# Kernel optimization log

Hardware: AMD Instinct MI355X
Metric: run time of the kernel (lower is better)

## Reference

```python
import jax, jax.numpy as jnp
import numpy as np
import math

B, S, DIM, H = 4, 1024, 4096, 32
HD = DIM // H  # head_dim = 128
MAX_B, MAX_S = 4, 1024
START_POS = 0
ROPE_THETA = 10000.0


def setup_inputs() -> dict:
    key = jax.random.key(0)
    ks = jax.random.split(key, 6)
    x = jax.random.normal(ks[0], (B, S, DIM), dtype=jnp.float32)
    # real RoPE frequencies: freqs_cis[t, j] = exp(i * t * theta^{-2j/hd})
    inv_freq = 1.0 / (ROPE_THETA ** (jnp.arange(0, HD, 2, dtype=jnp.float32) / HD))  # [HD/2]
    t = jnp.arange(START_POS, START_POS + S, dtype=jnp.float32)
    ang = jnp.outer(t, inv_freq)  # [S, HD/2]
    freqs_cos = jnp.cos(ang)
    freqs_sin = jnp.sin(ang)
    # additive causal mask as in llama: -inf above diagonal offset start_pos+1
    mask = jnp.triu(jnp.full((1, 1, S, S), float('-inf'), dtype=jnp.float32), k=START_POS + 1)
    scale = 0.02
    wq = jax.random.normal(ks[1], (DIM, DIM), dtype=jnp.float32) * scale
    wk = jax.random.normal(ks[2], (DIM, DIM), dtype=jnp.float32) * scale
    wv = jax.random.normal(ks[3], (DIM, DIM), dtype=jnp.float32) * scale
    wo = jax.random.normal(ks[4], (DIM, DIM), dtype=jnp.float32) * scale
    cache_k = jnp.zeros((MAX_B, MAX_S, H, HD), dtype=jnp.float32)
    cache_v = jnp.zeros((MAX_B, MAX_S, H, HD), dtype=jnp.float32)
    return {"x": x, "start_pos": START_POS, "freqs_cos": freqs_cos, "freqs_sin": freqs_sin,
            "mask": mask, "wq": wq, "wk": wk, "wv": wv, "wo": wo,
            "cache_k": cache_k, "cache_v": cache_v}


def _apply_rotary(t, cos, sin):
    # t: [B, S, H, HD]; interpret last dim as HD/2 complex pairs (real, imag)
    b, s, h, d = t.shape
    tr = t.reshape(b, s, h, d // 2, 2)
    a, bb = tr[..., 0], tr[..., 1]
    c = cos[None, :, None, :]  # [1, S, 1, HD/2]
    si = sin[None, :, None, :]
    out_r = a * c - bb * si
    out_i = a * si + bb * c
    return jnp.stack([out_r, out_i], axis=-1).reshape(b, s, h, d)


def reference(x, start_pos, freqs_cos, freqs_sin, mask, wq, wk, wv, wo, cache_k, cache_v):
    bsz, seqlen, dim = x.shape
    hd = HD
    # torch Linear: y = x @ W.T, W is [out, in]
    xq = (x @ wq.T).reshape(bsz, seqlen, H, hd)
    xk = (x @ wk.T).reshape(bsz, seqlen, H, hd)
    xv = (x @ wv.T).reshape(bsz, seqlen, H, hd)
    xq = _apply_rotary(xq, freqs_cos, freqs_sin)
    xk = _apply_rotary(xk, freqs_cos, freqs_sin)
    # KV-cache write
    cache_k = jax.lax.dynamic_update_slice(cache_k, xk, (0, start_pos, 0, 0))
    cache_v = jax.lax.dynamic_update_slice(cache_v, xv, (0, start_pos, 0, 0))
    keys = cache_k[:bsz, :start_pos + seqlen]    # [B, K, H, HD]
    values = cache_v[:bsz, :start_pos + seqlen]  # [B, K, H, HD]
    # naive attention: full score matrix
    scores = jnp.einsum('bqhd,bkhd->bhqk', xq, keys) / math.sqrt(hd)
    scores = scores + mask
    probs = jax.nn.softmax(scores.astype(jnp.float32), axis=-1).astype(xq.dtype)
    out = jnp.einsum('bhqk,bkhd->bqhd', probs, values)
    out = out.reshape(bsz, seqlen, -1)
    return out @ wo.T
```

## Files before the change

kernel.cpp:

```cpp
#include <hip/hip_runtime.h>
#include <hip/hip_bf16.h>
#include <cstdint>

typedef __hip_bfloat16 bf16;
typedef __attribute__((ext_vector_type(8))) short frag8;
typedef __attribute__((ext_vector_type(4))) float f32x4;

#define DEV __device__ __forceinline__

DEV void gl_lds16(const void* g, void* l) {
  __builtin_amdgcn_global_load_lds(
      (const __attribute__((address_space(1))) void*)g,
      (__attribute__((address_space(3))) void*)l, 16, 0, 0);
}

DEV void storeC(float* C, size_t idx, float v) { C[idx] = v; }
DEV void storeC(bf16* C, size_t idx, float v) { C[idx] = __float2bfloat16(v); }

__global__ __launch_bounds__(256) void conv_all(const float* __restrict__ x,
                                                const float* __restrict__ wq,
                                                const float* __restrict__ wk,
                                                const float* __restrict__ wv,
                                                const float* __restrict__ wo,
                                                bf16* __restrict__ xb, bf16* __restrict__ qb,
                                                bf16* __restrict__ kb, bf16* __restrict__ vb,
                                                bf16* __restrict__ ob) {
  const float* src;
  bf16* dst;
  switch (blockIdx.y) {
    case 0: src = x;  dst = xb; break;
    case 1: src = wq; dst = qb; break;
    case 2: src = wk; dst = kb; break;
    case 3: src = wv; dst = vb; break;
    default: src = wo; dst = ob; break;
  }
  int i = blockIdx.x * 256 + threadIdx.x;
  const f32x4* in4 = reinterpret_cast<const f32x4*>(src);
  f32x4 a = __builtin_nontemporal_load(in4 + 2 * i);
  f32x4 b = __builtin_nontemporal_load(in4 + 2 * i + 1);
  union { frag8 v; bf16 h[8]; } u;
  u.h[0] = __float2bfloat16(a.x); u.h[1] = __float2bfloat16(a.y);
  u.h[2] = __float2bfloat16(a.z); u.h[3] = __float2bfloat16(a.w);
  u.h[4] = __float2bfloat16(b.x); u.h[5] = __float2bfloat16(b.y);
  u.h[6] = __float2bfloat16(b.z); u.h[7] = __float2bfloat16(b.w);
  __builtin_nontemporal_store(u.v, reinterpret_cast<frag8*>(dst + (size_t)i * 8));
}

#define MF(a, b, c) __builtin_amdgcn_mfma_f32_16x16x32_bf16(a, b, c, 0, 0, 0)

#define STAGE(isB, h, tt, bp) do {                                             \
    char* _d = lds + ((isB) * 65536) + ((((bp) * 2) + (h)) << 14);             \
    gl_lds16(((isB) ? gB : gA)[h][0] + (size_t)(tt) * 64, _d + ldsOff0);       \
    gl_lds16(((isB) ? gB : gA)[h][1] + (size_t)(tt) * 64, _d + ldsOff1);       \
  } while (0)

#define RDA(mi, ckk) (*(const frag8*)(ab + aRowB + (mi) * 2048 + (ckk)))
#define RDB(ni, ckk) (*(const frag8*)(bb + bRowB + (ni) * 2048 + (ckk)))

#define PHASE(p, SSTAGE, SWAIT) do {                                           \
    if ((p) == 0) {                                                            \
      b00 = RDB(0, ck0); b01 = RDB(0, ck1); b10 = RDB(1, ck0); b11 = RDB(1, ck1); \
      b20 = RDB(2, ck0); b21 = RDB(2, ck1); b30 = RDB(3, ck0); b31 = RDB(3, ck1); \
    }                                                                          \
    frag8 a00 = RDA(2 * (p), ck0), a01 = RDA(2 * (p), ck1);                    \
    frag8 a10 = RDA(2 * (p) + 1, ck0), a11 = RDA(2 * (p) + 1, ck1);            \
    SSTAGE;                                                                    \
    SWAIT;                                                                     \
    __builtin_amdgcn_s_barrier();                                              \
    __builtin_amdgcn_s_setprio(1);                                             \
    acc[2*(p)][0]   = MF(a00, b00, acc[2*(p)][0]);                             \
    acc[2*(p)][1]   = MF(a00, b10, acc[2*(p)][1]);                             \
    acc[2*(p)][2]   = MF(a00, b20, acc[2*(p)][2]);                             \
    acc[2*(p)][3]   = MF(a00, b30, acc[2*(p)][3]);                             \
    acc[2*(p)+1][0] = MF(a10, b00, acc[2*(p)+1][0]);                           \
    acc[2*(p)+1][1] = MF(a10, b10, acc[2*(p)+1][1]);                           \
    acc[2*(p)+1][2] = MF(a10, b20, acc[2*(p)+1][2]);                           \
    acc[2*(p)+1][3] = MF(a10, b30, acc[2*(p)+1][3]);                           \
    acc[2*(p)][0]   = MF(a01, b01, acc[2*(p)][0]);                             \
    acc[2*(p)][1]   = MF(a01, b11, acc[2*(p)][1]);                             \
    acc[2*(p)][2]   = MF(a01, b21, acc[2*(p)][2]);                             \
    acc[2*(p)][3]   = MF(a01, b31, acc[2*(p)][3]);                             \
    acc[2*(p)+1][0] = MF(a11, b01, acc[2*(p)+1][0]);                           \
    acc[2*(p)+1][1] = MF(a11, b11, acc[2*(p)+1][1]);                           \
    acc[2*(p)+1][2] = MF(a11, b21, acc[2*(p)+1][2]);                           \
    acc[2*(p)+1][3] = MF(a11, b31, acc[2*(p)+1][3]);                           \
    __builtin_amdgcn_s_setprio(0);                                             \
    __builtin_amdgcn_s_barrier();                                              \
  } while (0)

#define VM4 asm volatile("s_waitcnt vmcnt(4)" ::: "memory")
#define VM0 asm volatile("s_waitcnt vmcnt(0)" ::: "memory")
#define NOW ((void)0)

#define TILE(t, SA, SB, SWAIT) do {                                            \
    const int _bp2 = ((t) & 1) * 2;                                            \
    char* ab = lds + ((_bp2 + wm) << 14);                                      \
    char* bb = lds + 65536 + ((_bp2 + bhalf) << 14);                           \
    PHASE(0, { if (SA) STAGE(0, 0, (t) + 1, ((t) + 1) & 1); }, NOW);           \
    PHASE(1, { if (SA) STAGE(0, 1, (t) + 1, ((t) + 1) & 1); }, NOW);           \
    PHASE(2, { if (SB) STAGE(1, 0, (t) + 2, (t) & 1); }, NOW);                 \
    PHASE(3, { if (SB) STAGE(1, 1, (t) + 2, (t) & 1); }, SWAIT);               \
  } while (0)

template <typename OutT, int EPI>
__global__ __launch_bounds__(512, 2) void gemm8(const bf16* __restrict__ A,
                                                const bf16* __restrict__ Bt,
                                                OutT* __restrict__ C,
                                                const float* __restrict__ fc,
                                                const float* __restrict__ fs,
                                                float oscale) {
  __shared__ __align__(16) char lds[131072];
  const int K = 4096, N = 4096;
  const int t = threadIdx.x;
  const int lane = t & 63, w = t >> 6;
  const int wm = w >> 2, wn = w & 3;
  const int lr = lane & 15, lg = lane >> 4;
  const int bhalf = wn >> 1;

  const int bid = blockIdx.x;
  const int wg = (bid & 7) * 32 + (bid >> 3);
  const int m0 = (wg >> 4) * 256, n0 = (wg & 15) * 256;

  const bf16* gA[2][2];
  const bf16* gB[2][2];
  int ldsOff0, ldsOff1;
  {
    int c0 = (w * 2 + 0) * 64 + lane;
    int c1 = (w * 2 + 1) * 64 + lane;
    int r0 = c0 >> 3, r1 = c1 >> 3;
    int e0 = ((c0 & 7) ^ (r0 & 7)) * 8;
    int e1 = ((c1 & 7) ^ (r1 & 7)) * 8;
    ldsOff0 = c0 * 16; ldsOff1 = c1 * 16;
    gA[0][0] = A + (size_t)(m0 + r0) * K + e0;
    gA[0][1] = A + (size_t)(m0 + r1) * K + e1;
    gA[1][0] = A + (size_t)(m0 + 128 + r0) * K + e0;
    gA[1][1] = A + (size_t)(m0 + 128 + r1) * K + e1;
    gB[0][0] = Bt + (size_t)(n0 + r0) * K + e0;
    gB[0][1] = Bt + (size_t)(n0 + r1) * K + e1;
    gB[1][0] = Bt + (size_t)(n0 + 128 + r0) * K + e0;
    gB[1][1] = Bt + (size_t)(n0 + 128 + r1) * K + e1;
  }

  const int swz = (lr & 7) << 4;
  const int ck0 = (lg * 16) ^ swz;
  const int ck1 = (64 + lg * 16) ^ swz;
  const int aRowB = lr * 128;
  const int bRowB = ((wn & 1) * 64 + lr) * 128;

  f32x4 acc[8][4];
#pragma unroll
  for (int mi = 0; mi < 8; ++mi)
#pragma unroll
    for (int ni = 0; ni < 4; ++ni) acc[mi][ni] = (f32x4){0.f, 0.f, 0.f, 0.f};

  frag8 b00, b01, b10, b11, b20, b21, b30, b31;

  STAGE(1, 0, 0, 0); STAGE(1, 1, 0, 0);
  STAGE(0, 0, 0, 0); STAGE(0, 1, 0, 0);
  STAGE(1, 0, 1, 1); STAGE(1, 1, 1, 1);
  VM4;
  __builtin_amdgcn_s_barrier();

  for (int tt = 0; tt < 62; tt += 2) {
    TILE(tt, 1, 1, VM4);
    TILE(tt + 1, 1, 1, VM4);
  }
  TILE(62, 1, 0, VM0);
  TILE(63, 0, 0, NOW);

#pragma unroll
  for (int mi = 0; mi < 8; ++mi)
#pragma unroll
    for (int ni = 0; ni < 4; ++ni) {
      f32x4 v = acc[mi][ni];
      int col = n0 + wn * 64 + ni * 16 + lr;
      if (EPI == 1) {
        int i = (col & 127) >> 1;
        const bool odd = (col & 1);
#pragma unroll
        for (int ii = 0; ii < 4; ++ii) {
          int row = m0 + wm * 128 + mi * 16 + lg * 4 + ii;
          int s = row & 1023;
          float c = fc[s * 64 + i], si = fs[s * 64 + i];
          float val = v[ii];
          float par = __shfl_xor(val, 1);
          float o = (val * c + (odd ? par * si : -par * si)) * oscale;
          storeC(C, (size_t)row * N + col, o);
        }
      } else if (EPI == 2) {
        int row0 = m0 + wm * 128 + mi * 16 + lg * 4;
        size_t base = ((size_t)(row0 >> 10) * 4096 + col) * 1024 + (row0 & 1023);
        union { ushort4 s4; unsigned short us[4]; } pk;
#pragma unroll
        for (int ii = 0; ii < 4; ++ii) {
          union { bf16 b; unsigned short u; } cv;
          cv.b = __float2bfloat16(v[ii]);
          pk.us[ii] = cv.u;
        }
        *reinterpret_cast<ushort4*>(reinterpret_cast<bf16*>(C) + base) = pk.s4;
      } else {
#pragma unroll
        for (int ii = 0; ii < 4; ++ii) {
          int row = m0 + wm * 128 + mi * 16 + lg * 4 + ii;
          storeC(C, (size_t)row * N + col, v[ii]);
        }
      }
    }
}

__global__ __launch_bounds__(512, 4) void attn_kernel(const bf16* __restrict__ q,
                                                      const bf16* __restrict__ k,
                                                      const bf16* __restrict__ vt,
                                                      bf16* __restrict__ out) {
  __shared__ __align__(16) char als[81920];
  const int qt = 7 - blockIdx.x, h = blockIdx.y, b = blockIdx.z;
  const int t = threadIdx.x;
  const int lane = t & 63, w = t >> 6;
  const int lr = lane & 15, lg = lane >> 4;
  const int NT = 2 * qt + 2;

  frag8 aq[4];
  {
    const bf16* qp = q + ((size_t)(b * 1024 + qt * 128 + w * 16 + lr)) * 4096 + h * 128 + lg * 8;
#pragma unroll
    for (int ks = 0; ks < 4; ++ks) aq[ks] = *reinterpret_cast<const frag8*>(qp + ks * 32);
  }

  const bf16* kbase = k + (size_t)b * 1024 * 4096 + h * 128;
  const bf16* vbase = vt + ((size_t)(b * 32 + h)) * 128 * 1024;

  const int L0 = t * 16, L1 = (t + 512) * 16;
  const int kr0 = L0 >> 8, kr1 = L1 >> 8;
  const size_t kOff0 = (size_t)kr0 * 4096 + (((L0 & 255) ^ ((kr0 & 7) << 4)) >> 1);
  const size_t kOff1 = (size_t)kr1 * 4096 + (((L1 & 255) ^ ((kr1 & 7) << 4)) >> 1);
  const int vr0 = L0 >> 7, vr1 = L1 >> 7;
  const size_t vOff0 = (size_t)vr0 * 1024 + (((L0 & 127) ^ ((vr0 & 7) << 4)) >> 1);
  const size_t vOff1 = (size_t)vr1 * 1024 + (((L1 & 127) ^ ((vr1 & 7) << 4)) >> 1);

#define STAGE_K(tt, bp) do { char* _d = als + (bp) * 16384;                    \
    gl_lds16(kbase + (size_t)(tt) * 262144 + kOff0, _d + L0);                  \
    gl_lds16(kbase + (size_t)(tt) * 262144 + kOff1, _d + L1); } while (0)
#define STAGE_V(tt, bp) do { char* _d = als + 32768 + (bp) * 16384;            \
    gl_lds16(vbase + (size_t)(tt) * 64 + vOff0, _d + L0);                      \
    gl_lds16(vbase + (size_t)(tt) * 64 + vOff1, _d + L1); } while (0)

  f32x4 oacc[8] = {};
  float mrow = -1e30f, lrow = 0.f;
  char* Pw = als + 65536 + w * 2048;
  const int qmaxw = qt * 128 + w * 16 + 15;
  const int qr_g = qt * 128 + w * 16 + lr;

  STAGE_K(0, 0); STAGE_V(0, 0);
  STAGE_K(1, 1); STAGE_V(1, 1);

  for (int kt = 0; kt < NT; ++kt) {
    const int cur = kt & 1;
    const bool act = (kt * 64 <= qmaxw);
    const bool domask = (kt >= 2 * qt);
    char* Kc = als + cur * 16384;
    char* Vc = als + 32768 + cur * 16384;

    if (kt + 1 < NT) { VM4; } else { VM0; }
    __builtin_amdgcn_s_barrier();

    f32x4 sacc[4] = {};
    if (act) {
      __builtin_amdgcn_s_setprio(1);
#pragma unroll
      for (int ks = 0; ks < 4; ++ks) {
#pragma unroll
        for (int ni = 0; ni < 4; ++ni) {
          int n = ni * 16 + lr;
          frag8 bk = *reinterpret_cast<const frag8*>(
              Kc + n * 256 + ((ks * 64 + lg * 16) ^ ((n & 7) << 4)));
          sacc[ni] = MF(bk, aq[ks], sacc[ni]);
        }
      }
      __builtin_amdgcn_s_setprio(0);
    }
    __builtin_amdgcn_s_barrier();
    if (kt + 2 < NT) STAGE_K(kt + 2, cur);

    if (act) {
      if (domask) {
#pragma unroll
        for (int ni = 0; ni < 4; ++ni)
#pragma unroll
          for (int i = 0; i < 4; ++i) {
            int kc = kt * 64 + ni * 16 + lg * 4 + i;
            if (kc > qr_g) sacc[ni][i] = -1e30f;
          }
      }

      float pm = sacc[0][0];
#pragma unroll
      for (int ni = 0; ni < 4; ++ni)
#pragma unroll
        for (int i = 0; i < 4; ++i) pm = fmaxf(pm, sacc[ni][i]);
      pm = fmaxf(pm, __shfl_xor(pm, 16));
      pm = fmaxf(pm, __shfl_xor(pm, 32));
      const bool skip = __all(pm <= mrow + 8.f);
      float mn, f;
      if (skip) { mn = mrow; f = 1.f; }
      else      { mn = fmaxf(mrow, pm); f = __expf(mrow - mn); mrow = mn; }
      float rs = 0.f;
#pragma unroll
      for (int ni = 0; ni < 4; ++ni)
#pragma unroll
        for (int i = 0; i < 4; ++i) {
          float p = __expf(sacc[ni][i] - mn);
          sacc[ni][i] = p;
          rs += p;
        }
      rs += __shfl_xor(rs, 16);
      rs += __shfl_xor(rs, 32);
      lrow = lrow * f + rs;

#pragma unroll
      for (int ni = 0; ni < 4; ++ni)
#pragma unroll
        for (int jj = 0; jj < 2; ++jj) {
          union { uint32_t u; bf16 hh[2]; } pk;
          pk.hh[0] = __float2bfloat16(sacc[ni][2 * jj]);
          pk.hh[1] = __float2bfloat16(sacc[ni][2 * jj + 1]);
          int kc2 = (ni * 16 + lg * 4 + 2 * jj) * 2;
          *reinterpret_cast<uint32_t*>(Pw + lr * 128 + (kc2 ^ ((lr & 7) << 4))) = pk.u;
        }

      if (!skip) {
        float fi0 = __shfl(f, lg * 4 + 0);
        float fi1 = __shfl(f, lg * 4 + 1);
        float fi2 = __shfl(f, lg * 4 + 2);
        float fi3 = __shfl(f, lg * 4 + 3);
#pragma unroll
        for (int nj = 0; nj < 8; ++nj) {
          oacc[nj][0] *= fi0; oacc[nj][1] *= fi1;
          oacc[nj][2] *= fi2; oacc[nj][3] *= fi3;
        }
      }

      __builtin_amdgcn_s_setprio(1);
#pragma unroll
      for (int ks2 = 0; ks2 < 2; ++ks2) {
        frag8 ap = *reinterpret_cast<const frag8*>(
            Pw + lr * 128 + ((ks2 * 64 + lg * 16) ^ ((lr & 7) << 4)));
#pragma unroll
        for (int nj = 0; nj < 8; ++nj) {
          int d = nj * 16 + lr;
          frag8 bv = *reinterpret_cast<const frag8*>(
              Vc + d * 128 + ((ks2 * 64 + lg * 16) ^ ((d & 7) << 4)));
          oacc[nj] = MF(ap, bv, oacc[nj]);
        }
      }
      __builtin_amdgcn_s_setprio(0);
    }
    __builtin_amdgcn_s_barrier();
    if (kt + 2 < NT) STAGE_V(kt + 2, cur);
  }

  float lv0 = __shfl(lrow, lg * 4 + 0);
  float lv1 = __shfl(lrow, lg * 4 + 1);
  float lv2 = __shfl(lrow, lg * 4 + 2);
  float lv3 = __shfl(lrow, lg * 4 + 3);
#pragma unroll
  for (int nj = 0; nj < 8; ++nj) {
    int srow0 = qt * 128 + w * 16 + lg * 4;
    size_t base = ((size_t)(b * 1024 + srow0)) * 4096 + h * 128 + nj * 16 + lr;
    out[base]          = __float2bfloat16(oacc[nj][0] / lv0);
    out[base + 4096]   = __float2bfloat16(oacc[nj][1] / lv1);
    out[base + 8192]   = __float2bfloat16(oacc[nj][2] / lv2);
    out[base + 12288]  = __float2bfloat16(oacc[nj][3] / lv3);
  }
#undef STAGE_K
#undef STAGE_V
}

extern "C" void kernel_launch(void* const* d_in, const int* in_sizes, int n_in,
                              void* d_out, int out_size, void* d_ws, size_t ws_size,
                              hipStream_t stream) {
  const float* x  = (const float*)d_in[0];
  const float* fc = (const float*)d_in[2];
  const float* fs = (const float*)d_in[3];
  const float* wq = (const float*)d_in[5];
  const float* wk = (const float*)d_in[6];
  const float* wv = (const float*)d_in[7];
  const float* wo = (const float*)d_in[8];
  float* out = (float*)d_out;

  const size_t SZ = (size_t)4096 * 4096 * 2;
  char* w = (char*)d_ws;
  bf16* xb  = (bf16*)(w);
  bf16* wbq = (bf16*)(w + SZ);
  bf16* qb  = (bf16*)(w + 2 * SZ);
  bf16* kb  = (bf16*)(w + 3 * SZ);
  bf16* vtb = (bf16*)(w + 4 * SZ);
  bf16* wbk = (bf16*)(w + 5 * SZ);
  bf16* wbv = (bf16*)(w + 6 * SZ);
  bf16* wbo = (bf16*)(w + 7 * SZ);
  bf16* ao  = xb;

  const int n8 = 4096 * 4096 / 8;
  dim3 cgrd(n8 / 256, 5), blk(256);
  dim3 ggrd(256);
  dim3 gblk(512);

  conv_all<<<cgrd, blk, 0, stream>>>(x, wq, wk, wv, wo, xb, wbq, wbk, wbv, wbo);
  gemm8<bf16, 1><<<ggrd, gblk, 0, stream>>>(xb, wbq, qb, fc, fs, 0.08838834764831845f);
  gemm8<bf16, 1><<<ggrd, gblk, 0, stream>>>(xb, wbk, kb, fc, fs, 1.0f);
  gemm8<bf16, 2><<<ggrd, gblk, 0, stream>>>(xb, wbv, vtb, fc, fs, 1.0f);
  attn_kernel<<<dim3(8, 32, 4), gblk, 0, stream>>>(qb, kb, vtb, ao);
  gemm8<float, 0><<<ggrd, gblk, 0, stream>>>(ao, wbo, out, fc, fs, 1.0f);
}
```

Before: 638.0 us.

## Triple-buffer A tiles in GEMM to prefetch two K-steps ahead

The bf16 GEMM previously double-buffered both A and B in LDS and prefetched A only one K-tile ahead. A now uses a three-slot LDS ring and is prefetched two tiles ahead, matching B, with the vmcnt wait raised from 4 to 8 to allow more outstanding global-to-LDS loads. This aims to hide more global load latency behind the MFMA work. In exchange, LDS per block grows from 128 KB to 160 KB, and the ring index needs a runtime modulo-3. The attention kernel keeps its old wait count under a renamed macro.

```diff
diff --git a/kernel.cpp b/kernel.cpp
--- a/kernel.cpp
+++ b/kernel.cpp
@@ -48,10 +48,15 @@
 
 #define MF(a, b, c) __builtin_amdgcn_mfma_f32_16x16x32_bf16(a, b, c, 0, 0, 0)
 
-#define STAGE(isB, h, tt, bp) do {                                             \
-    char* _d = lds + ((isB) * 65536) + ((((bp) * 2) + (h)) << 14);             \
-    gl_lds16(((isB) ? gB : gA)[h][0] + (size_t)(tt) * 64, _d + ldsOff0);       \
-    gl_lds16(((isB) ? gB : gA)[h][1] + (size_t)(tt) * 64, _d + ldsOff1);       \
+#define STAGE_A(h, tt, bp3) do {                                               \
+    char* _d = lds + ((bp3) * 32768) + ((h) << 14);                            \
+    gl_lds16(gA[h][0] + (size_t)(tt) * 64, _d + ldsOff0);                      \
+    gl_lds16(gA[h][1] + (size_t)(tt) * 64, _d + ldsOff1);                      \
+  } while (0)
+#define STAGE_B(h, tt, bp2) do {                                               \
+    char* _d = lds + 98304 + ((bp2) * 32768) + ((h) << 14);                    \
+    gl_lds16(gB[h][0] + (size_t)(tt) * 64, _d + ldsOff0);                      \
+    gl_lds16(gB[h][1] + (size_t)(tt) * 64, _d + ldsOff1);                      \
   } while (0)
 
 #define RDA(mi, ckk) (*(const frag8*)(ab + aRowB + (mi) * 2048 + (ckk)))
@@ -88,18 +93,17 @@
     __builtin_amdgcn_s_barrier();                                              \
   } while (0)
 
-#define VM4 asm volatile("s_waitcnt vmcnt(4)" ::: "memory")
+#define VM8 asm volatile("s_waitcnt vmcnt(8)" ::: "memory")
 #define VM0 asm volatile("s_waitcnt vmcnt(0)" ::: "memory")
 #define NOW ((void)0)
 
 #define TILE(t, SA, SB, SWAIT) do {                                            \
-    const int _bp2 = ((t) & 1) * 2;                                            \
-    char* ab = lds + ((_bp2 + wm) << 14);                                      \
-    char* bb = lds + 65536 + ((_bp2 + bhalf) << 14);                           \
-    PHASE(0, { if (SA) STAGE(0, 0, (t) + 1, ((t) + 1) & 1); }, NOW);           \
-    PHASE(1, { if (SA) STAGE(0, 1, (t) + 1, ((t) + 1) & 1); }, NOW);           \
-    PHASE(2, { if (SB) STAGE(1, 0, (t) + 2, (t) & 1); }, NOW);                 \
-    PHASE(3, { if (SB) STAGE(1, 1, (t) + 2, (t) & 1); }, SWAIT);               \
+    char* ab = lds + ((t) % 3) * 32768 + (wm << 14);                           \
+    char* bb = lds + 98304 + (((t) & 1) * 32768) + (bhalf << 14);              \
+    PHASE(0, { if (SA) STAGE_A(0, (t) + 2, ((t) + 2) % 3); }, NOW);            \
+    PHASE(1, { if (SA) STAGE_A(1, (t) + 2, ((t) + 2) % 3); }, NOW);            \
+    PHASE(2, { if (SB) STAGE_B(0, (t) + 2, (t) & 1); }, NOW);                  \
+    PHASE(3, { if (SB) STAGE_B(1, (t) + 2, (t) & 1); }, SWAIT);                \
   } while (0)
 
 template <typename OutT, int EPI>
@@ -109,7 +113,7 @@
                                                 const float* __restrict__ fc,
                                                 const float* __restrict__ fs,
                                                 float oscale) {
-  __shared__ __align__(16) char lds[131072];
+  __shared__ __align__(16) char lds[163840];
   const int K = 4096, N = 4096;
   const int t = threadIdx.x;
   const int lane = t & 63, w = t >> 6;
@@ -155,17 +159,18 @@
 
   frag8 b00, b01, b10, b11, b20, b21, b30, b31;
 
-  STAGE(1, 0, 0, 0); STAGE(1, 1, 0, 0);
-  STAGE(0, 0, 0, 0); STAGE(0, 1, 0, 0);
-  STAGE(1, 0, 1, 1); STAGE(1, 1, 1, 1);
-  VM4;
+  STAGE_A(0, 0, 0); STAGE_A(1, 0, 0);
+  STAGE_B(0, 0, 0); STAGE_B(1, 0, 0);
+  STAGE_A(0, 1, 1); STAGE_A(1, 1, 1);
+  STAGE_B(0, 1, 1); STAGE_B(1, 1, 1);
+  VM8;
   __builtin_amdgcn_s_barrier();
 
   for (int tt = 0; tt < 62; tt += 2) {
-    TILE(tt, 1, 1, VM4);
-    TILE(tt + 1, 1, 1, VM4);
-  }
-  TILE(62, 1, 0, VM0);
+    TILE(tt, 1, 1, VM8);
+    TILE(tt + 1, 1, 1, VM8);
+  }
+  TILE(62, 0, 0, VM0);
   TILE(63, 0, 0, NOW);
 
 #pragma unroll
@@ -244,6 +249,8 @@
     gl_lds16(vbase + (size_t)(tt) * 64 + vOff0, _d + L0);                      \
     gl_lds16(vbase + (size_t)(tt) * 64 + vOff1, _d + L1); } while (0)
 
+#define VM4A asm volatile("s_waitcnt vmcnt(4)" ::: "memory")
+
   f32x4 oacc[8] = {};
   float mrow = -1e30f, lrow = 0.f;
   char* Pw = als + 65536 + w * 2048;
@@ -260,7 +267,7 @@
     char* Kc = als + cur * 16384;
     char* Vc = als + 32768 + cur * 16384;
 
-    if (kt + 1 < NT) { VM4; } else { VM0; }
+    if (kt + 1 < NT) { VM4A; } else { VM0; }
     __builtin_amdgcn_s_barrier();
 
     f32x4 sacc[4] = {};
```

New measurement: 642.8 us. No clear change (+0.8%).

## Fuse Q, K, V projection GEMMs into one launch over concatenated weights

Applied to the files above, without the earlier changes.

Lays the converted wq, wk and wv bf16 weights out contiguously and runs a single 768-block GEMM covering a 4096x12288 output. Each block selects Q, K or V from its column tile and applies the matching epilogue: rotary plus scale for Q, rotary for K, transposed store for V. This removes two launches and the tail/idle gaps between them, and fills the GPU with more concurrent blocks. The cost is extra per-block index arithmetic and a branchier epilogue.

```diff
diff --git a/kernel.cpp b/kernel.cpp
--- a/kernel.cpp
+++ b/kernel.cpp
@@ -106,6 +106,8 @@
 __global__ __launch_bounds__(512, 2) void gemm8(const bf16* __restrict__ A,
                                                 const bf16* __restrict__ Bt,
                                                 OutT* __restrict__ C,
+                                                bf16* __restrict__ Ck,
+                                                bf16* __restrict__ Cv,
                                                 const float* __restrict__ fc,
                                                 const float* __restrict__ fs,
                                                 float oscale) {
@@ -118,8 +120,18 @@
   const int bhalf = wn >> 1;
 
   const int bid = blockIdx.x;
-  const int wg = (bid & 7) * 32 + (bid >> 3);
-  const int m0 = (wg >> 4) * 256, n0 = (wg & 15) * 256;
+  int m0, n0g;
+  if (EPI == 3) {
+    const int wg = (bid & 7) * 96 + (bid >> 3);
+    m0 = (wg / 48) * 256;
+    n0g = (wg % 48) * 256;
+  } else {
+    const int wg = (bid & 7) * 32 + (bid >> 3);
+    m0 = (wg >> 4) * 256;
+    n0g = (wg & 15) * 256;
+  }
+  const int wsel = (EPI == 3) ? (n0g >> 12) : 0;
+  const int n0 = (EPI == 3) ? (n0g & 4095) : n0g;
 
   const bf16* gA[2][2];
   const bf16* gB[2][2];
@@ -135,10 +147,10 @@
     gA[0][1] = A + (size_t)(m0 + r1) * K + e1;
     gA[1][0] = A + (size_t)(m0 + 128 + r0) * K + e0;
     gA[1][1] = A + (size_t)(m0 + 128 + r1) * K + e1;
-    gB[0][0] = Bt + (size_t)(n0 + r0) * K + e0;
-    gB[0][1] = Bt + (size_t)(n0 + r1) * K + e1;
-    gB[1][0] = Bt + (size_t)(n0 + 128 + r0) * K + e0;
-    gB[1][1] = Bt + (size_t)(n0 + 128 + r1) * K + e1;
+    gB[0][0] = Bt + (size_t)(n0g + r0) * K + e0;
+    gB[0][1] = Bt + (size_t)(n0g + r1) * K + e1;
+    gB[1][0] = Bt + (size_t)(n0g + 128 + r0) * K + e0;
+    gB[1][1] = Bt + (size_t)(n0g + 128 + r1) * K + e1;
   }
 
   const int swz = (lr & 7) << 4;
@@ -174,30 +186,34 @@
     for (int ni = 0; ni < 4; ++ni) {
       f32x4 v = acc[mi][ni];
       int col = n0 + wn * 64 + ni * 16 + lr;
-      if (EPI == 1) {
-        int i = (col & 127) >> 1;
-        const bool odd = (col & 1);
-#pragma unroll
-        for (int ii = 0; ii < 4; ++ii) {
-          int row = m0 + wm * 128 + mi * 16 + lg * 4 + ii;
-          int s = row & 1023;
-          float c = fc[s * 64 + i], si = fs[s * 64 + i];
-          float val = v[ii];
-          float par = __shfl_xor(val, 1);
-          float o = (val * c + (odd ? par * si : -par * si)) * oscale;
-          storeC(C, (size_t)row * N + col, o);
-        }
-      } else if (EPI == 2) {
-        int row0 = m0 + wm * 128 + mi * 16 + lg * 4;
-        size_t base = ((size_t)(row0 >> 10) * 4096 + col) * 1024 + (row0 & 1023);
-        union { ushort4 s4; unsigned short us[4]; } pk;
-#pragma unroll
-        for (int ii = 0; ii < 4; ++ii) {
-          union { bf16 b; unsigned short u; } cv;
-          cv.b = __float2bfloat16(v[ii]);
-          pk.us[ii] = cv.u;
-        }
-        *reinterpret_cast<ushort4*>(reinterpret_cast<bf16*>(C) + base) = pk.s4;
+      if (EPI == 3) {
+        if (wsel < 2) {
+          bf16* Cd = wsel ? Ck : reinterpret_cast<bf16*>(C);
+          const float os = wsel ? 1.0f : 0.08838834764831845f;
+          int i = (col & 127) >> 1;
+          const bool odd = (col & 1);
+#pragma unroll
+          for (int ii = 0; ii < 4; ++ii) {
+            int row = m0 + wm * 128 + mi * 16 + lg * 4 + ii;
+            int s = row & 1023;
+            float c = fc[s * 64 + i], si = fs[s * 64 + i];
+            float val = v[ii];
+            float par = __shfl_xor(val, 1);
+            float o = (val * c + (odd ? par * si : -par * si)) * os;
+            Cd[(size_t)row * N + col] = __float2bfloat16(o);
+          }
+        } else {
+          int row0 = m0 + wm * 128 + mi * 16 + lg * 4;
+          size_t base = ((size_t)(row0 >> 10) * 4096 + col) * 1024 + (row0 & 1023);
+          union { ushort4 s4; unsigned short us[4]; } pk;
+#pragma unroll
+          for (int ii = 0; ii < 4; ++ii) {
+            union { bf16 b; unsigned short u; } cv;
+            cv.b = __float2bfloat16(v[ii]);
+            pk.us[ii] = cv.u;
+          }
+          *reinterpret_cast<ushort4*>(Cv + base) = pk.s4;
+        }
       } else {
 #pragma unroll
         for (int ii = 0; ii < 4; ++ii) {
@@ -388,26 +404,23 @@
   float* out = (float*)d_out;
 
   const size_t SZ = (size_t)4096 * 4096 * 2;
+  const size_t NE = (size_t)4096 * 4096;
   char* w = (char*)d_ws;
-  bf16* xb  = (bf16*)(w);
-  bf16* wbq = (bf16*)(w + SZ);
-  bf16* qb  = (bf16*)(w + 2 * SZ);
-  bf16* kb  = (bf16*)(w + 3 * SZ);
-  bf16* vtb = (bf16*)(w + 4 * SZ);
-  bf16* wbk = (bf16*)(w + 5 * SZ);
-  bf16* wbv = (bf16*)(w + 6 * SZ);
-  bf16* wbo = (bf16*)(w + 7 * SZ);
-  bf16* ao  = xb;
+  bf16* xb   = (bf16*)(w);
+  bf16* wbo  = (bf16*)(w + SZ);
+  bf16* qb   = (bf16*)(w + 2 * SZ);
+  bf16* kb   = (bf16*)(w + 3 * SZ);
+  bf16* vtb  = (bf16*)(w + 4 * SZ);
+  bf16* wqkv = (bf16*)(w + 5 * SZ);
+  bf16* ao   = xb;
 
   const int n8 = 4096 * 4096 / 8;
   dim3 cgrd(n8 / 256, 5), blk(256);
-  dim3 ggrd(256);
   dim3 gblk(512);
 
-  conv_all<<<cgrd, blk, 0, stream>>>(x, wq, wk, wv, wo, xb, wbq, wbk, wbv, wbo);
-  gemm8<bf16, 1><<<ggrd, gblk, 0, stream>>>(xb, wbq, qb, fc, fs, 0.08838834764831845f);
-  gemm8<bf16, 1><<<ggrd, gblk, 0, stream>>>(xb, wbk, kb, fc, fs, 1.0f);
-  gemm8<bf16, 2><<<ggrd, gblk, 0, stream>>>(xb, wbv, vtb, fc, fs, 1.0f);
+  conv_all<<<cgrd, blk, 0, stream>>>(x, wq, wk, wv, wo,
+                                     xb, wqkv, wqkv + NE, wqkv + 2 * NE, wbo);
+  gemm8<bf16, 3><<<dim3(768), gblk, 0, stream>>>(xb, wqkv, qb, kb, vtb, fc, fs, 1.0f);
   attn_kernel<<<dim3(8, 32, 4), gblk, 0, stream>>>(qb, kb, vtb, ao);
-  gemm8<float, 0><<<ggrd, gblk, 0, stream>>>(ao, wbo, out, fc, fs, 1.0f);
+  gemm8<float, 0><<<dim3(256), gblk, 0, stream>>>(ao, wbo, out, nullptr, nullptr, fc, fs, 1.0f);
 }
```

After: 645.5 us. No clear change (+1.2%).
